# Kernel optimization log

Hardware: AMD Instinct MI355X
Metric: run time of the kernel (lower is better)

The kernel has to match this reference:

```python
import jax, jax.numpy as jnp
import numpy as np

N_NODES = 50000
N_EDGES = 800000
IN_DIM = 128
HID_DIM = 128


def gcn_conv(x, edge_index, W, b):
    # PyG GCNConv: out = D^{-1/2} (A + I) D^{-1/2} X W + b
    n = x.shape[0]
    loop = jnp.arange(n)
    src = jnp.concatenate([edge_index[0], loop])
    dst = jnp.concatenate([edge_index[1], loop])
    deg = jax.ops.segment_sum(jnp.ones_like(dst, dtype=x.dtype), dst, num_segments=n)
    dinv = jax.lax.rsqrt(jnp.maximum(deg, 1.0))  # deg >= 1 with self-loops
    norm = dinv[src] * dinv[dst]                 # [E+N]
    h = x @ W                                    # [N, out_dim] dense transform first (smaller msgs)
    msg = h[src] * norm[:, None]                 # gather + scale
    return jax.ops.segment_sum(msg, dst, num_segments=n) + b  # scatter-add


def gcn_backbone(x, edge_index, W0, b0, W1, b1):
    h = jax.nn.relu(gcn_conv(x, edge_index, W0, b0))
    return gcn_conv(h, edge_index, W1, b1)


def setup_inputs() -> dict:
    key = jax.random.key(0)
    ks = jax.random.split(key, 8)
    s_in = 1.0 / np.sqrt(IN_DIM)
    s_h = 1.0 / np.sqrt(HID_DIM)
    return {
        "x1": jax.random.normal(ks[0], (N_NODES, IN_DIM), dtype=jnp.float32),
        "edge_index1": jax.random.randint(ks[1], (2, N_EDGES), 0, N_NODES, dtype=jnp.int32),
        "x2": jax.random.normal(ks[2], (N_NODES, IN_DIM), dtype=jnp.float32),
        "edge_index2": jax.random.randint(ks[3], (2, N_EDGES), 0, N_NODES, dtype=jnp.int32),
        "W0": jax.random.normal(ks[4], (IN_DIM, HID_DIM), dtype=jnp.float32) * s_in,
        "b0": jnp.zeros((HID_DIM,), dtype=jnp.float32),
        "W1": jax.random.normal(ks[5], (HID_DIM, HID_DIM), dtype=jnp.float32) * s_h,
        "b1": jnp.zeros((HID_DIM,), dtype=jnp.float32),
    }


def reference(x1, edge_index1, x2, edge_index2, W0, b0, W1, b1):
    z1 = gcn_backbone(x1, edge_index1, W0, b0, W1, b1)
    z2 = gcn_backbone(x2, edge_index2, W0, b0, W1, b1)
    return (z1, z2)
```

## Files before the change

### kernel.cpp

```cpp
#include <hip/hip_runtime.h>

#define GN 50000
#define GE 800000
#define GD 128
#define CAP 64
#define NBIN 8
#define BINW 6250
#define NCHUNK 400

typedef unsigned short u16;
typedef unsigned int u32;
typedef short bf16x8 __attribute__((ext_vector_type(8)));
typedef float f32x4 __attribute__((ext_vector_type(4)));
typedef u16 u16x8 __attribute__((ext_vector_type(8)));
typedef u16 u16x4 __attribute__((ext_vector_type(4)));

__device__ inline float bf2f_lo(u32 u) {
  union { u32 i; float f; } v; v.i = u << 16; return v.f;
}
__device__ inline float bf2f_hi(u32 u) {
  union { u32 i; float f; } v; v.i = u & 0xffff0000u; return v.f;
}
__device__ inline u16 f2bf(float f) {
  union { float f; u32 i; } v; v.f = f;
  u32 r = v.i + 0x7fffu + ((v.i >> 16) & 1u);
  return (u16)(r >> 16);
}
__device__ inline float rlf(float v, int l) {
  return __int_as_float(__builtin_amdgcn_readlane(__float_as_int(v), l));
}

__global__ __launch_bounds__(256) void k_build(const int* __restrict__ e1,
                                               const int* __restrict__ e2,
                                               int* __restrict__ cnt,
                                               u16* __restrict__ bucket) {
  const int half = NBIN * NCHUNK;
  int gb = blockIdx.x >= half;
  int bid = blockIdx.x - gb * half;
  const int* E = gb ? e2 : e1;
  const int* src = E;
  const int* dst = E + GE;
  int* c = cnt + gb * GN;
  u16* bk = bucket + (size_t)gb * GN * CAP;

  int bin = bid & (NBIN - 1);
  int chunk = bid >> 3;
  int t0 = chunk * 256 + threadIdx.x;
  const int stride = NCHUNK * 256;
  int lo = bin * BINW, hi = lo + BINW;

  int s[8], d[8];
#pragma unroll
  for (int k = 0; k < 8; k++) {
    int e = t0 + k * stride;
    int ec = (e < GE) ? e : 0;
    s[k] = __builtin_nontemporal_load(&src[ec]);
    d[k] = __builtin_nontemporal_load(&dst[ec]);
    if (e >= GE) d[k] = -1;
  }
#pragma unroll
  for (int k = 0; k < 8; k++) {
    if (d[k] >= lo && d[k] < hi) {
      int slot = atomicAdd(&c[d[k]], 1);
      if (slot < CAP) bk[d[k] * CAP + slot] = (u16)s[k];
    }
  }
}

__global__ __launch_bounds__(256) void k_dinv(const int* __restrict__ cnt,
                                              float* __restrict__ dinv) {
  int i = blockIdx.x * 256 + threadIdx.x;
  if (i >= 2 * GN) return;
  dinv[i] = rsqrtf((float)(cnt[i] + 1));
}

__global__ __launch_bounds__(256) void k_prep(const float* __restrict__ W0,
                                              const float* __restrict__ W1,
                                              u16* __restrict__ Wf0,
                                              u16* __restrict__ Wf1) {
  int idx = blockIdx.x * 256 + threadIdx.x;
  const float* W = (idx & 2048) ? W1 : W0;
  u16* Wf = (idx & 2048) ? Wf1 : Wf0;
  int r = idx & 2047;
  int kq = r >> 9, cb = (r >> 6) & 7, lane = r & 63;
  int m16 = lane & 15, quad = lane >> 4;
  int k0 = kq * 32 + quad * 8;
  int n = cb * 16 + m16;
  u16x8 o;
#pragma unroll
  for (int j = 0; j < 8; j++) o[j] = f2bf(W[(k0 + j) * 128 + n]);
  *(u16x8*)&Wf[((kq * 8 + cb) * 64 + lane) * 8] = o;
}

#define NB ((GN + 63) / 64)
template <bool IN_F32>
__global__ __launch_bounds__(256, 4) void k_gemm(const void* __restrict__ X1,
                                                 const void* __restrict__ X2,
                                                 const u16* __restrict__ Wf,
                                                 u16* __restrict__ H) {
  __shared__ u16 Xs[64][136];
  int gb = blockIdx.x >= NB;
  int bid = blockIdx.x - gb * NB;
  const void* Xin = gb ? X2 : X1;
  u16* Hh = H + (size_t)gb * GN * GD;

  int t = threadIdx.x;
  int lane = t & 63, wave = t >> 6;
  int m16 = lane & 15, quad = lane >> 4;
  int r0 = bid * 64;

  bf16x8 bfr[4][2];
#pragma unroll
  for (int kq = 0; kq < 4; kq++)
#pragma unroll
    for (int c = 0; c < 2; c++)
      bfr[kq][c] = *(const bf16x8*)&Wf[((kq * 8 + wave * 2 + c) * 64 + lane) * 8];

  if (IN_F32) {
    const float4* Xv = (const float4*)Xin;
#pragma unroll
    for (int i = 0; i < 8; i++) {
      int idx = i * 256 + t;
      int row = idx >> 5, c4 = idx & 31;
      int gr = r0 + row; if (gr >= GN) gr = GN - 1;
      float4 v = Xv[(size_t)gr * 32 + c4];
      u16x4 u; u.x = f2bf(v.x); u.y = f2bf(v.y); u.z = f2bf(v.z); u.w = f2bf(v.w);
      *(u16x4*)&Xs[row][c4 * 4] = u;
    }
  } else {
    const u16x8* Xv = (const u16x8*)Xin;
#pragma unroll
    for (int i = 0; i < 4; i++) {
      int idx = i * 256 + t;
      int row = idx >> 4, c8 = idx & 15;
      int gr = r0 + row; if (gr >= GN) gr = GN - 1;
      *(u16x8*)&Xs[row][c8 * 8] = Xv[(size_t)gr * 16 + c8];
    }
  }
  __syncthreads();

  f32x4 acc[4][2] = {};
#pragma unroll
  for (int kq = 0; kq < 4; kq++) {
#pragma unroll
    for (int rb = 0; rb < 4; rb++) {
      bf16x8 a = *(const bf16x8*)&Xs[rb * 16 + m16][kq * 32 + quad * 8];
      acc[rb][0] = __builtin_amdgcn_mfma_f32_16x16x32_bf16(a, bfr[kq][0], acc[rb][0], 0, 0, 0);
      acc[rb][1] = __builtin_amdgcn_mfma_f32_16x16x32_bf16(a, bfr[kq][1], acc[rb][1], 0, 0, 0);
    }
  }

#pragma unroll
  for (int rb = 0; rb < 4; rb++) {
#pragma unroll
    for (int i = 0; i < 4; i++) {
      int grow = r0 + rb * 16 + quad * 4 + i;
      if (grow < GN) {
#pragma unroll
        for (int c = 0; c < 2; c++)
          Hh[(size_t)grow * 128 + (wave * 2 + c) * 16 + m16] = f2bf(acc[rb][c][i]);
      }
    }
  }
}

template <bool FINAL>
__global__ __launch_bounds__(256) void k_agg(const u16* __restrict__ H,
                                             const u16* __restrict__ bucket,
                                             const int* __restrict__ cnt,
                                             const float* __restrict__ dinv,
                                             const float* __restrict__ bias,
                                             void* __restrict__ out) {
  int widg = (blockIdx.x * 256 + threadIdx.x) >> 6;
  int lane = threadIdx.x & 63;
  if (widg >= 2 * GN) return;
  int gb = widg >= GN;
  int wid = widg - gb * GN;

  const int* c = cnt + gb * GN;
  const float* dvp = dinv + gb * GN;
  const u16* bk = bucket + (size_t)gb * GN * CAP;
  const u32* Hv = (const u32*)H + (size_t)gb * GN * 64;

  float dv = dvp[wid];
  int deg = min(c[wid], CAP);

  int s_l = 0;
  float d_l = 0.f;
  if (lane < deg) {
    s_l = (int)bk[wid * CAP + lane];
    d_l = dvp[s_l];
  }

  u32 hs = Hv[(size_t)wid * 64 + lane];
  float ax = dv * bf2f_lo(hs);
  float ay = dv * bf2f_hi(hs);
  float2 bb = ((const float2*)bias)[lane];

  int dpad = (deg + 15) & ~15;
  for (int i = 0; i < dpad; i += 16) {
    int ss[16];
    u32 hh[16];
    float ww[16];
#pragma unroll
    for (int j = 0; j < 16; j++) ss[j] = __builtin_amdgcn_readlane(s_l, i + j);
#pragma unroll
    for (int j = 0; j < 16; j++) hh[j] = Hv[(size_t)ss[j] * 64 + lane];
#pragma unroll
    for (int j = 0; j < 16; j++) ww[j] = rlf(d_l, i + j);
#pragma unroll
    for (int j = 0; j < 16; j++) {
      ax += ww[j] * bf2f_lo(hh[j]);
      ay += ww[j] * bf2f_hi(hh[j]);
    }
  }

  float ox = dv * ax + bb.x;
  float oy = dv * ay + bb.y;
  if (!FINAL) {
    ox = fmaxf(ox, 0.f); oy = fmaxf(oy, 0.f);
    u32 packed = ((u32)f2bf(oy) << 16) | (u32)f2bf(ox);
    ((u32*)out)[(size_t)widg * 64 + lane] = packed;
  } else {
    ((float2*)out)[(size_t)widg * 64 + lane] = make_float2(ox, oy);
  }
}

extern "C" void kernel_launch(void* const* d_in, const int* in_sizes, int n_in,
                              void* d_out, int out_size, void* d_ws, size_t ws_size,
                              hipStream_t stream) {
  const float* x1 = (const float*)d_in[0];
  const int* ei1  = (const int*)d_in[1];
  const float* x2 = (const float*)d_in[2];
  const int* ei2  = (const int*)d_in[3];
  const float* W0 = (const float*)d_in[4];
  const float* b0 = (const float*)d_in[5];
  const float* W1 = (const float*)d_in[6];
  const float* b1 = (const float*)d_in[7];
  float* out = (float*)d_out;

  char* ws = (char*)d_ws;
  size_t off = 0;
  auto carve = [&](size_t bytes) -> char* {
    char* p = ws + off;
    off = (off + bytes + 511) & ~(size_t)511;
    return p;
  };
  int* cnt    = (int*)carve((size_t)2 * GN * 4);
  float* dinv = (float*)carve((size_t)2 * GN * 4);
  u16* bucket = (u16*)carve((size_t)2 * GN * CAP * 2);
  u16* h      = (u16*)carve((size_t)2 * GN * GD * 2);
  u16* a      = (u16*)carve((size_t)2 * GN * GD * 2);
  u16* W0f    = (u16*)carve((size_t)GD * GD * 2);
  u16* W1f    = (u16*)carve((size_t)GD * GD * 2);

  k_prep<<<16, 256, 0, stream>>>(W0, W1, W0f, W1f);
  hipMemsetAsync(cnt, 0, (size_t)2 * GN * 4, stream);
  k_build<<<2 * NBIN * NCHUNK, 256, 0, stream>>>(ei1, ei2, cnt, bucket);
  k_dinv<<<(2 * GN + 255) / 256, 256, 0, stream>>>(cnt, dinv);

  k_gemm<true><<<2 * NB, 256, 0, stream>>>(x1, x2, W0f, h);
  k_agg<false><<<(2 * GN * 64 + 255) / 256, 256, 0, stream>>>(h, bucket, cnt, dinv, b0, a);

  k_gemm<false><<<2 * NB, 256, 0, stream>>>(a, a + (size_t)GN * GD, W1f, h);
  k_agg<true><<<(2 * GN * 64 + 255) / 256, 256, 0, stream>>>(h, bucket, cnt, dinv, b1, out);
}
```

Before: 326.1 us.

## Fuse CSR build with first GEMM, fold memset and dinv into other kernels

Merges the edge-bucketing kernel and the first dense transform into one launch, with blocks picking their role by index so the memory-bound atomics and the MFMA GEMM can share the GPU at the same time. The counter memset is folded into the weight-prep kernel, and the separate dinv kernel and buffer are removed: aggregation now computes rsqrt(deg+1) on the fly from the counts. This cuts launches and a pass over memory, at the cost of an extra dependent gather of c[src] per neighbour in aggregation, plus shared-memory allocation on build blocks that do not use it.

```diff
diff --git a/kernel.cpp b/kernel.cpp
--- a/kernel.cpp
+++ b/kernel.cpp
@@ -30,78 +30,83 @@
   return __int_as_float(__builtin_amdgcn_readlane(__float_as_int(v), l));
 }
 
-__global__ __launch_bounds__(256) void k_build(const int* __restrict__ e1,
-                                               const int* __restrict__ e2,
-                                               int* __restrict__ cnt,
-                                               u16* __restrict__ bucket) {
-  const int half = NBIN * NCHUNK;
-  int gb = blockIdx.x >= half;
-  int bid = blockIdx.x - gb * half;
-  const int* E = gb ? e2 : e1;
-  const int* src = E;
-  const int* dst = E + GE;
-  int* c = cnt + gb * GN;
-  u16* bk = bucket + (size_t)gb * GN * CAP;
-
-  int bin = bid & (NBIN - 1);
-  int chunk = bid >> 3;
-  int t0 = chunk * 256 + threadIdx.x;
-  const int stride = NCHUNK * 256;
-  int lo = bin * BINW, hi = lo + BINW;
-
-  int s[8], d[8];
-#pragma unroll
-  for (int k = 0; k < 8; k++) {
-    int e = t0 + k * stride;
-    int ec = (e < GE) ? e : 0;
-    s[k] = __builtin_nontemporal_load(&src[ec]);
-    d[k] = __builtin_nontemporal_load(&dst[ec]);
-    if (e >= GE) d[k] = -1;
-  }
-#pragma unroll
-  for (int k = 0; k < 8; k++) {
-    if (d[k] >= lo && d[k] < hi) {
-      int slot = atomicAdd(&c[d[k]], 1);
-      if (slot < CAP) bk[d[k] * CAP + slot] = (u16)s[k];
-    }
-  }
-}
-
-__global__ __launch_bounds__(256) void k_dinv(const int* __restrict__ cnt,
-                                              float* __restrict__ dinv) {
-  int i = blockIdx.x * 256 + threadIdx.x;
-  if (i >= 2 * GN) return;
-  dinv[i] = rsqrtf((float)(cnt[i] + 1));
-}
+#define NB ((GN + 63) / 64)
+#define GEMM_BLKS (2 * NB)
+#define BUILD_BLKS (2 * NBIN * NCHUNK)
 
 __global__ __launch_bounds__(256) void k_prep(const float* __restrict__ W0,
                                               const float* __restrict__ W1,
                                               u16* __restrict__ Wf0,
-                                              u16* __restrict__ Wf1) {
+                                              u16* __restrict__ Wf1,
+                                              int* __restrict__ cnt) {
   int idx = blockIdx.x * 256 + threadIdx.x;
-  const float* W = (idx & 2048) ? W1 : W0;
-  u16* Wf = (idx & 2048) ? Wf1 : Wf0;
-  int r = idx & 2047;
-  int kq = r >> 9, cb = (r >> 6) & 7, lane = r & 63;
-  int m16 = lane & 15, quad = lane >> 4;
-  int k0 = kq * 32 + quad * 8;
-  int n = cb * 16 + m16;
-  u16x8 o;
-#pragma unroll
-  for (int j = 0; j < 8; j++) o[j] = f2bf(W[(k0 + j) * 128 + n]);
-  *(u16x8*)&Wf[((kq * 8 + cb) * 64 + lane) * 8] = o;
-}
-
-#define NB ((GN + 63) / 64)
-template <bool IN_F32>
-__global__ __launch_bounds__(256, 4) void k_gemm(const void* __restrict__ X1,
-                                                 const void* __restrict__ X2,
-                                                 const u16* __restrict__ Wf,
-                                                 u16* __restrict__ H) {
+  if (idx < 4096) {
+    const float* W = (idx & 2048) ? W1 : W0;
+    u16* Wf = (idx & 2048) ? Wf1 : Wf0;
+    int r = idx & 2047;
+    int kq = r >> 9, cb = (r >> 6) & 7, lane = r & 63;
+    int m16 = lane & 15, quad = lane >> 4;
+    int k0 = kq * 32 + quad * 8;
+    int n = cb * 16 + m16;
+    u16x8 o;
+#pragma unroll
+    for (int j = 0; j < 8; j++) o[j] = f2bf(W[(k0 + j) * 128 + n]);
+    *(u16x8*)&Wf[((kq * 8 + cb) * 64 + lane) * 8] = o;
+  } else {
+    int z = idx - 4096;
+    if (z < 2 * GN) cnt[z] = 0;
+  }
+}
+
+__global__ __launch_bounds__(256, 4) void k_fused1(const int* __restrict__ e1,
+                                                   const int* __restrict__ e2,
+                                                   int* __restrict__ cnt,
+                                                   u16* __restrict__ bucket,
+                                                   const float* __restrict__ X1,
+                                                   const float* __restrict__ X2,
+                                                   const u16* __restrict__ Wf,
+                                                   u16* __restrict__ H) {
   __shared__ u16 Xs[64][136];
+
+  if (blockIdx.x >= GEMM_BLKS) {
+    int b = blockIdx.x - GEMM_BLKS;
+    const int half = NBIN * NCHUNK;
+    int gb = b >= half;
+    int bid = b - gb * half;
+    const int* E = gb ? e2 : e1;
+    const int* src = E;
+    const int* dst = E + GE;
+    int* c = cnt + gb * GN;
+    u16* bk = bucket + (size_t)gb * GN * CAP;
+
+    int bin = bid & (NBIN - 1);
+    int chunk = bid >> 3;
+    int t0 = chunk * 256 + threadIdx.x;
+    const int stride = NCHUNK * 256;
+    int lo = bin * BINW, hi = lo + BINW;
+
+    int s[8], d[8];
+#pragma unroll
+    for (int k = 0; k < 8; k++) {
+      int e = t0 + k * stride;
+      int ec = (e < GE) ? e : 0;
+      s[k] = __builtin_nontemporal_load(&src[ec]);
+      d[k] = __builtin_nontemporal_load(&dst[ec]);
+      if (e >= GE) d[k] = -1;
+    }
+#pragma unroll
+    for (int k = 0; k < 8; k++) {
+      if (d[k] >= lo && d[k] < hi) {
+        int slot = atomicAdd(&c[d[k]], 1);
+        if (slot < CAP) bk[d[k] * CAP + slot] = (u16)s[k];
+      }
+    }
+    return;
+  }
+
   int gb = blockIdx.x >= NB;
   int bid = blockIdx.x - gb * NB;
-  const void* Xin = gb ? X2 : X1;
+  const float* Xin = gb ? X2 : X1;
   u16* Hh = H + (size_t)gb * GN * GD;
 
   int t = threadIdx.x;
@@ -116,7 +121,7 @@
     for (int c = 0; c < 2; c++)
       bfr[kq][c] = *(const bf16x8*)&Wf[((kq * 8 + wave * 2 + c) * 64 + lane) * 8];
 
-  if (IN_F32) {
+  {
     const float4* Xv = (const float4*)Xin;
 #pragma unroll
     for (int i = 0; i < 8; i++) {
@@ -127,7 +132,57 @@
       u16x4 u; u.x = f2bf(v.x); u.y = f2bf(v.y); u.z = f2bf(v.z); u.w = f2bf(v.w);
       *(u16x4*)&Xs[row][c4 * 4] = u;
     }
-  } else {
+  }
+  __syncthreads();
+
+  f32x4 acc[4][2] = {};
+#pragma unroll
+  for (int kq = 0; kq < 4; kq++) {
+#pragma unroll
+    for (int rb = 0; rb < 4; rb++) {
+      bf16x8 a = *(const bf16x8*)&Xs[rb * 16 + m16][kq * 32 + quad * 8];
+      acc[rb][0] = __builtin_amdgcn_mfma_f32_16x16x32_bf16(a, bfr[kq][0], acc[rb][0], 0, 0, 0);
+      acc[rb][1] = __builtin_amdgcn_mfma_f32_16x16x32_bf16(a, bfr[kq][1], acc[rb][1], 0, 0, 0);
+    }
+  }
+
+#pragma unroll
+  for (int rb = 0; rb < 4; rb++) {
+#pragma unroll
+    for (int i = 0; i < 4; i++) {
+      int grow = r0 + rb * 16 + quad * 4 + i;
+      if (grow < GN) {
+#pragma unroll
+        for (int c = 0; c < 2; c++)
+          Hh[(size_t)grow * 128 + (wave * 2 + c) * 16 + m16] = f2bf(acc[rb][c][i]);
+      }
+    }
+  }
+}
+
+__global__ __launch_bounds__(256, 4) void k_gemm2(const u16* __restrict__ X1,
+                                                  const u16* __restrict__ X2,
+                                                  const u16* __restrict__ Wf,
+                                                  u16* __restrict__ H) {
+  __shared__ u16 Xs[64][136];
+  int gb = blockIdx.x >= NB;
+  int bid = blockIdx.x - gb * NB;
+  const u16* Xin = gb ? X2 : X1;
+  u16* Hh = H + (size_t)gb * GN * GD;
+
+  int t = threadIdx.x;
+  int lane = t & 63, wave = t >> 6;
+  int m16 = lane & 15, quad = lane >> 4;
+  int r0 = bid * 64;
+
+  bf16x8 bfr[4][2];
+#pragma unroll
+  for (int kq = 0; kq < 4; kq++)
+#pragma unroll
+    for (int c = 0; c < 2; c++)
+      bfr[kq][c] = *(const bf16x8*)&Wf[((kq * 8 + wave * 2 + c) * 64 + lane) * 8];
+
+  {
     const u16x8* Xv = (const u16x8*)Xin;
 #pragma unroll
     for (int i = 0; i < 4; i++) {
@@ -168,7 +223,6 @@
 __global__ __launch_bounds__(256) void k_agg(const u16* __restrict__ H,
                                              const u16* __restrict__ bucket,
                                              const int* __restrict__ cnt,
-                                             const float* __restrict__ dinv,
                                              const float* __restrict__ bias,
                                              void* __restrict__ out) {
   int widg = (blockIdx.x * 256 + threadIdx.x) >> 6;
@@ -178,18 +232,18 @@
   int wid = widg - gb * GN;
 
   const int* c = cnt + gb * GN;
-  const float* dvp = dinv + gb * GN;
   const u16* bk = bucket + (size_t)gb * GN * CAP;
   const u32* Hv = (const u32*)H + (size_t)gb * GN * 64;
 
-  float dv = dvp[wid];
-  int deg = min(c[wid], CAP);
+  int cw = c[wid];
+  float dv = rsqrtf((float)(cw + 1));
+  int deg = min(cw, CAP);
 
   int s_l = 0;
   float d_l = 0.f;
   if (lane < deg) {
     s_l = (int)bk[wid * CAP + lane];
-    d_l = dvp[s_l];
+    d_l = rsqrtf((float)(c[s_l] + 1));
   }
 
   u32 hs = Hv[(size_t)wid * 64 + lane];
@@ -247,21 +301,20 @@
     return p;
   };
   int* cnt    = (int*)carve((size_t)2 * GN * 4);
-  float* dinv = (float*)carve((size_t)2 * GN * 4);
   u16* bucket = (u16*)carve((size_t)2 * GN * CAP * 2);
   u16* h      = (u16*)carve((size_t)2 * GN * GD * 2);
   u16* a      = (u16*)carve((size_t)2 * GN * GD * 2);
   u16* W0f    = (u16*)carve((size_t)GD * GD * 2);
   u16* W1f    = (u16*)carve((size_t)GD * GD * 2);
 
-  k_prep<<<16, 256, 0, stream>>>(W0, W1, W0f, W1f);
-  hipMemsetAsync(cnt, 0, (size_t)2 * GN * 4, stream);
-  k_build<<<2 * NBIN * NCHUNK, 256, 0, stream>>>(ei1, ei2, cnt, bucket);
-  k_dinv<<<(2 * GN + 255) / 256, 256, 0, stream>>>(cnt, dinv);
-
-  k_gemm<true><<<2 * NB, 256, 0, stream>>>(x1, x2, W0f, h);
-  k_agg<false><<<(2 * GN * 64 + 255) / 256, 256, 0, stream>>>(h, bucket, cnt, dinv, b0, a);
-
-  k_gemm<false><<<2 * NB, 256, 0, stream>>>(a, a + (size_t)GN * GD, W1f, h);
-  k_agg<true><<<(2 * GN * 64 + 255) / 256, 256, 0, stream>>>(h, bucket, cnt, dinv, b1, out);
-}
+  k_prep<<<(4096 + 2 * GN + 255) / 256, 256, 0, stream>>>(W0, W1, W0f, W1f, cnt);
+
+  k_fused1<<<GEMM_BLKS + BUILD_BLKS, 256, 0, stream>>>(ei1, ei2, cnt, bucket,
+                                                       x1, x2, W0f, h);
+
+  k_agg<false><<<(2 * GN * 64 + 255) / 256, 256, 0, stream>>>(h, bucket, cnt, b0, a);
+
+  k_gemm2<<<2 * NB, 256, 0, stream>>>(a, a + (size_t)GN * GD, W1f, h);
+
+  k_agg<true><<<(2 * GN * 64 + 255) / 256, 256, 0, stream>>>(h, bucket, cnt, b1, out);
+}
```

Result: faster. 318.6 us (-2.3%).
